# Optimization experiments

Measured on AMD Instinct MI355X. Metric: run time of the kernel, lower is better.

## Reference

```python
import jax, jax.numpy as jnp
import numpy as np

B, H, Wd = 32, 64, 64
C_IN = 65            # ambient Lorentz dim (1 time + 64 space)
KH = KW = 3          # kernel
OUT = 256            # out_channels (ambient); linear space dim = 255
HCAT = (C_IN - 1) * KH * KW + 1  # 577
CURV = 1.0


def setup_inputs() -> dict:
    key = jax.random.key(0)
    k1, k2, k3 = jax.random.split(key, 3)
    # spatial (tangent-like) components, projected onto the hyperboloid
    v = jax.random.normal(k1, (B, H, Wd, C_IN - 1), dtype=jnp.float32) * 0.5
    t = jnp.sqrt(1.0 / CURV + jnp.sum(v * v, axis=-1, keepdims=True))
    x = jnp.concatenate([t, v], axis=-1)  # valid Lorentz points, (B,H,W,65)
    W = jax.random.normal(k2, (OUT - 1, HCAT), dtype=jnp.float32) * (1.0 / np.sqrt(HCAT))
    b = jnp.zeros((OUT - 1,), dtype=jnp.float32)
    return {"x": x, "W": W, "b": b}


def reference(x, W, b):
    c = CURV
    Bn, Hn, Wn, C = x.shape
    # 'SAME' padding with stride 1, kernel 3 -> pad 1 on each side, edge mode
    xp = jnp.pad(x, ((0, 0), (1, 1), (1, 1), (0, 0)), mode="edge")
    # im2col: stack the KH*KW shifted views -> (B, H, W, N, C)
    slabs = [xp[:, i:i + Hn, j:j + Wn, :] for i in range(KH) for j in range(KW)]
    patches = jnp.stack(slabs, axis=3)
    N = KH * KW
    # Lorentz direct concatenation (HCat):
    # time = sqrt(sum_i t_i^2 - (N-1)/c), space = concat of spatial parts
    t_cat = jnp.sqrt(jnp.sum(patches[..., 0] ** 2, axis=-1) - (N - 1) / c)
    sp = patches[..., 1:].reshape(Bn, Hn, Wn, N * (C - 1))
    h = jnp.concatenate([t_cat[..., None], sp], axis=-1)  # (B,H,W,577)
    # Hyperbolic linear (Lorentz fully-connected): space part is affine map,
    # time part restores the Lorentz constraint <y,y>_L = -1/c
    z = jnp.einsum("bhwi,oi->bhwo", h, W) + b  # (B,H,W,255)
    t_out = jnp.sqrt(1.0 / c + jnp.sum(z * z, axis=-1, keepdims=True))
    return jnp.concatenate([t_out, z], axis=-1)  # (B,H,W,256)
```

## Files before the change

kernel.cpp:

```cpp
#include <hip/hip_runtime.h>
#include <hip/hip_bf16.h>


#define CLAMP63(v) ((v) < 0 ? 0 : ((v) > 63 ? 63 : (v)))

typedef __attribute__((ext_vector_type(8))) short short8;
typedef __attribute__((ext_vector_type(4))) float floatx4;

__device__ __forceinline__ void gl2lds16(const void* g, void* l) {
  __builtin_amdgcn_global_load_lds(
      (const __attribute__((address_space(1))) void*)g,
      (__attribute__((address_space(3))) void*)l, 16, 0, 0);
}

__global__ void prep_x(const float* __restrict__ x, __hip_bfloat16* __restrict__ xs,
                       float* __restrict__ tsq) {
  int idx = blockIdx.x * 256 + threadIdx.x;
  int p = idx >> 3, g = idx & 7;
  const float* src = x + (size_t)p * 65 + 1 + g * 8;
  __align__(16) __hip_bfloat16 tmp[8];
#pragma unroll
  for (int i = 0; i < 8; ++i) tmp[i] = __float2bfloat16(src[i]);
  *(short8*)(xs + (size_t)idx * 8) = *(const short8*)tmp;
  if (g == 0) { float t = x[(size_t)p * 65]; tsq[p] = t * t; }
}

__global__ void prep_w(const float* __restrict__ W, const float* __restrict__ b,
                       __hip_bfloat16* __restrict__ Wb, float* __restrict__ Wt0,
                       float* __restrict__ bp) {
  int n = blockIdx.x;
  for (int k = threadIdx.x; k < 576; k += 256)
    Wb[n * 576 + k] = __float2bfloat16((n < 255) ? W[n * 577 + 1 + k] : 0.f);
  if (threadIdx.x == 0) {
    Wt0[n] = (n < 255) ? W[n * 577] : 0.f;
    bp[n]  = (n < 255) ? b[n] : 0.f;
  }
}

#define STAGE(IT, BUF)                                                          \
  do {                                                                          \
    const int nbr_ = (IT) >> 1;                                                 \
    const int dy_ = nbr_ / 3 - 1, dx_ = nbr_ % 3 - 1;                           \
    const int c0_ = ((IT) & 1) * 32;                                            \
    int y2_ = CLAMP63(a_by + dy_);                                              \
    int x2_ = CLAMP63(a_bx + dx_);                                              \
    gl2lds16(xs + (size_t)((a_bb * 64 + y2_) * 64 + x2_) * 64 + c0_ + a_kg * 8, \
             Ab + (BUF) * 4096 + w * 512);                                      \
    _Pragma("unroll")                                                           \
    for (int j = 0; j < 2; ++j)                                                 \
      gl2lds16(b_src[j] + (IT) * 32, Bb + (BUF) * 8192 + (w * 2 + j) * 512);    \
  } while (0)

__launch_bounds__(512, 4)
__global__ void hypconv_main(const float* __restrict__ tsq,
                             const __hip_bfloat16* __restrict__ xs,
                             const __hip_bfloat16* __restrict__ Wb,
                             const float* __restrict__ Wt0,
                             const float* __restrict__ bp,
                             float* __restrict__ out) {
  __shared__ __align__(16) char smem[49152];
  __shared__ float tc_lds[128];
  ushort* Ab = (ushort*)smem;
  ushort* Bb = (ushort*)(smem + 16384);
  float* zbuf = (float*)smem;

  const int tid = threadIdx.x;
  const int w = tid >> 6, lane = tid & 63;
  const int quad = lane >> 4, ln = lane & 15;
  const int pix_base = blockIdx.x * 128;
  const int m_off = (w >> 2) * 64, n_off = (w & 3) * 64;

  const int a_kg = w >> 1;
  int apix = pix_base + (w & 1) * 64 + lane;
  const int a_bx = apix & 63, a_by = (apix >> 6) & 63, a_bb = apix >> 12;
  const __hip_bfloat16* b_src[2];
#pragma unroll
  for (int j = 0; j < 2; ++j) {
    int c = w * 2 + j;
    b_src[j] = Wb + (size_t)((c & 3) * 64 + lane) * 576 + (c >> 2) * 8;
  }

  floatx4 acc[4][4];
#pragma unroll
  for (int mf = 0; mf < 4; ++mf)
#pragma unroll
    for (int nf = 0; nf < 4; ++nf)
      acc[mf][nf] = (floatx4){0.f, 0.f, 0.f, 0.f};

  STAGE(0, 0);

  if (tid < 128) {
    int pix = pix_base + tid;
    int bx = pix & 63, by = (pix >> 6) & 63, bb = pix >> 12;
    float s = 0.f;
#pragma unroll
    for (int dy = -1; dy <= 1; ++dy) {
      int y2 = CLAMP63(by + dy);
#pragma unroll
      for (int dx = -1; dx <= 1; ++dx) {
        int x2 = CLAMP63(bx + dx);
        s += tsq[(bb * 64 + y2) * 64 + x2];
      }
    }
    tc_lds[tid] = sqrtf(s - 8.0f);
  }

  for (int it = 0; it < 18; ++it) {
    __syncthreads();
    if (it < 17) STAGE(it + 1, (it + 1) & 1);
    const ushort* Ar = Ab + (it & 1) * 4096;
    const ushort* Br = Bb + (it & 1) * 8192;
    short8 af[4], bfr[4];
#pragma unroll
    for (int mf = 0; mf < 4; ++mf)
      af[mf] = *(const short8*)&Ar[(quad * 128 + m_off + mf * 16 + ln) * 8];
#pragma unroll
    for (int nf = 0; nf < 4; ++nf)
      bfr[nf] = *(const short8*)&Br[(quad * 256 + n_off + nf * 16 + ln) * 8];
#pragma unroll
    for (int mf = 0; mf < 4; ++mf)
#pragma unroll
      for (int nf = 0; nf < 4; ++nf)
        acc[mf][nf] = __builtin_amdgcn_mfma_f32_16x16x32_bf16(af[mf], bfr[nf], acc[mf][nf], 0, 0, 0);
  }

  __syncthreads();
  float wn[4], bnv[4];
#pragma unroll
  for (int nf = 0; nf < 4; ++nf) {
    int n = n_off + nf * 16 + ln;
    wn[nf] = Wt0[n];
    bnv[nf] = bp[n];
  }

#pragma unroll
  for (int mf = 0; mf < 4; ++mf) {
#pragma unroll
    for (int r = 0; r < 4; ++r) {
      float tcv = tc_lds[m_off + mf * 16 + quad * 4 + r];
      int lr = (w >> 2) * 16 + quad * 4 + r;
#pragma unroll
      for (int nf = 0; nf < 4; ++nf) {
        float z = acc[mf][nf][r] + bnv[nf] + tcv * wn[nf];
        zbuf[lr * 260 + ((1 + n_off + nf * 16 + ln) & 255)] = z;
      }
    }
    __syncthreads();
#pragma unroll
    for (int rr = 0; rr < 4; ++rr) {
      int lr = w * 4 + rr;
      float4 v = *(const float4*)&zbuf[lr * 260 + lane * 4];
      float ss = v.x * v.x + v.y * v.y + v.z * v.z + v.w * v.w;
      ss += __shfl_xor(ss, 1, 64);
      ss += __shfl_xor(ss, 2, 64);
      ss += __shfl_xor(ss, 4, 64);
      ss += __shfl_xor(ss, 8, 64);
      ss += __shfl_xor(ss, 16, 64);
      ss += __shfl_xor(ss, 32, 64);
      float tout = sqrtf(1.0f + ss);
      if (lane == 0) v.x = tout;
      int m = (lr >> 4) * 64 + mf * 16 + (lr & 15);
      *(float4*)&out[(size_t)(pix_base + m) * 256 + lane * 4] = v;
    }
    if (mf < 3) __syncthreads();
  }
}

extern "C" void kernel_launch(void* const* d_in, const int* in_sizes, int n_in,
                              void* d_out, int out_size, void* d_ws, size_t ws_size,
                              hipStream_t stream) {
  const float* x = (const float*)d_in[0];
  const float* W = (const float*)d_in[1];
  const float* b = (const float*)d_in[2];
  float* out = (float*)d_out;
  char* ws = (char*)d_ws;

  __hip_bfloat16* xs  = (__hip_bfloat16*)(ws);
  __hip_bfloat16* Wb  = (__hip_bfloat16*)(ws + 16777216);
  float*          Wt0 = (float*)(ws + 17072128);
  float*          bp  = (float*)(ws + 17073152);
  float*          tsq = (float*)(ws + 17074176);

  prep_x<<<4096, 256, 0, stream>>>(x, xs, tsq);
  prep_w<<<256,  256, 0, stream>>>(W, b, Wb, Wt0, bp);
  hypconv_main<<<1024, 512, 0, stream>>>(tsq, xs, Wb, Wt0, bp, out);
}
```

Before: 221.5 us.

## Fuse input bf16 conversion into main kernel with LDS halo tile

Removes the separate prep_x pass. Each block now loads a 4x66 halo of x straight from global memory, converts it to bf16 and stores it in LDS with an XOR swizzle, so the nine stencil neighbours are read from LDS and not re-fetched from global per iteration. The time-component sums also come from the LDS halo. It additionally remaps block order, shifts W rows by one so the output column layout needs no wrap, and lowers occupancy to 2 blocks per CU because LDS use grows. In exchange there are uncoalesced fp32 reads of 65-float rows and a larger LDS footprint per block.

```diff
diff --git a/kernel.cpp b/kernel.cpp
--- a/kernel.cpp
+++ b/kernel.cpp
@@ -13,66 +13,47 @@
       (__attribute__((address_space(3))) void*)l, 16, 0, 0);
 }
 
-__global__ void prep_x(const float* __restrict__ x, __hip_bfloat16* __restrict__ xs,
-                       float* __restrict__ tsq) {
-  int idx = blockIdx.x * 256 + threadIdx.x;
-  int p = idx >> 3, g = idx & 7;
-  const float* src = x + (size_t)p * 65 + 1 + g * 8;
-  __align__(16) __hip_bfloat16 tmp[8];
-#pragma unroll
-  for (int i = 0; i < 8; ++i) tmp[i] = __float2bfloat16(src[i]);
-  *(short8*)(xs + (size_t)idx * 8) = *(const short8*)tmp;
-  if (g == 0) { float t = x[(size_t)p * 65]; tsq[p] = t * t; }
-}
-
 __global__ void prep_w(const float* __restrict__ W, const float* __restrict__ b,
                        __hip_bfloat16* __restrict__ Wb, float* __restrict__ Wt0,
                        float* __restrict__ bp) {
   int n = blockIdx.x;
   for (int k = threadIdx.x; k < 576; k += 256)
-    Wb[n * 576 + k] = __float2bfloat16((n < 255) ? W[n * 577 + 1 + k] : 0.f);
+    Wb[n * 576 + k] = __float2bfloat16((n >= 1) ? W[(n - 1) * 577 + 1 + k] : 0.f);
   if (threadIdx.x == 0) {
-    Wt0[n] = (n < 255) ? W[n * 577] : 0.f;
-    bp[n]  = (n < 255) ? b[n] : 0.f;
+    Wt0[n] = (n >= 1) ? W[(n - 1) * 577] : 0.f;
+    bp[n]  = (n >= 1) ? b[n - 1] : 0.f;
   }
 }
 
-#define STAGE(IT, BUF)                                                          \
-  do {                                                                          \
-    const int nbr_ = (IT) >> 1;                                                 \
-    const int dy_ = nbr_ / 3 - 1, dx_ = nbr_ % 3 - 1;                           \
-    const int c0_ = ((IT) & 1) * 32;                                            \
-    int y2_ = CLAMP63(a_by + dy_);                                              \
-    int x2_ = CLAMP63(a_bx + dx_);                                              \
-    gl2lds16(xs + (size_t)((a_bb * 64 + y2_) * 64 + x2_) * 64 + c0_ + a_kg * 8, \
-             Ab + (BUF) * 4096 + w * 512);                                      \
-    _Pragma("unroll")                                                           \
-    for (int j = 0; j < 2; ++j)                                                 \
-      gl2lds16(b_src[j] + (IT) * 32, Bb + (BUF) * 8192 + (w * 2 + j) * 512);    \
+#define STAGE_B(IT, BUF)                                                          \
+  do {                                                                            \
+    _Pragma("unroll")                                                             \
+    for (int j_ = 0; j_ < 2; ++j_)                                                \
+      gl2lds16(b_src[j_] + (IT) * 32, Bb + (BUF) * 8192 + (w * 2 + j_) * 512);    \
   } while (0)
 
-__launch_bounds__(512, 4)
-__global__ void hypconv_main(const float* __restrict__ tsq,
-                             const __hip_bfloat16* __restrict__ xs,
+__launch_bounds__(512, 2)
+__global__ void hypconv_main(const float* __restrict__ x,
                              const __hip_bfloat16* __restrict__ Wb,
                              const float* __restrict__ Wt0,
                              const float* __restrict__ bp,
                              float* __restrict__ out) {
-  __shared__ __align__(16) char smem[49152];
+  __shared__ __align__(16) char smem[67616];
   __shared__ float tc_lds[128];
-  ushort* Ab = (ushort*)smem;
-  ushort* Bb = (ushort*)(smem + 16384);
+  float* ts = (float*)(smem + 33792);
+  ushort* Bb = (ushort*)(smem + 34848);
   float* zbuf = (float*)smem;
 
   const int tid = threadIdx.x;
   const int w = tid >> 6, lane = tid & 63;
   const int quad = lane >> 4, ln = lane & 15;
-  const int pix_base = blockIdx.x * 128;
+
+  const int mb = ((blockIdx.x & 7) << 7) + (blockIdx.x >> 3);
+  const int pix_base = mb * 128;
+  const int bb = mb >> 5;
+  const int r0 = (mb & 31) << 1;
   const int m_off = (w >> 2) * 64, n_off = (w & 3) * 64;
 
-  const int a_kg = w >> 1;
-  int apix = pix_base + (w & 1) * 64 + lane;
-  const int a_bx = apix & 63, a_by = (apix >> 6) & 63, a_bb = apix >> 12;
   const __hip_bfloat16* b_src[2];
 #pragma unroll
   for (int j = 0; j < 2; ++j) {
@@ -87,33 +68,54 @@
     for (int nf = 0; nf < 4; ++nf)
       acc[mf][nf] = (floatx4){0.f, 0.f, 0.f, 0.f};
 
-  STAGE(0, 0);
+  STAGE_B(0, 0);
+
+  for (int t = tid; t < 528; t += 512) {
+    const int hp = t >> 1, h = t & 1;
+    const int hyi = hp / 66, hxj = hp - hyi * 66;
+    const int gy = CLAMP63(r0 - 1 + hyi);
+    const int gx = CLAMP63(hxj - 1);
+    const float* row = x + (size_t)((bb << 12) + (gy << 6) + gx) * 65;
+    if (h == 0) { float tv = row[0]; ts[hp] = tv * tv; }
+    const float* sp = row + 1 + h * 32;
+#pragma unroll
+    for (int q = 0; q < 4; ++q) {
+      const int cg = h * 4 + q;
+      __align__(16) __hip_bfloat16 tmp[8];
+#pragma unroll
+      for (int i = 0; i < 8; ++i) tmp[i] = __float2bfloat16(sp[q * 8 + i]);
+      *(short8*)(smem + hp * 128 + ((cg ^ (hp & 7)) << 4)) = *(const short8*)tmp;
+    }
+  }
+  __syncthreads();
 
   if (tid < 128) {
-    int pix = pix_base + tid;
-    int bx = pix & 63, by = (pix >> 6) & 63, bb = pix >> 12;
+    const int ri = tid >> 6, cm = tid & 63;
     float s = 0.f;
 #pragma unroll
-    for (int dy = -1; dy <= 1; ++dy) {
-      int y2 = CLAMP63(by + dy);
+    for (int i = 0; i < 3; ++i)
 #pragma unroll
-      for (int dx = -1; dx <= 1; ++dx) {
-        int x2 = CLAMP63(bx + dx);
-        s += tsq[(bb * 64 + y2) * 64 + x2];
-      }
-    }
+      for (int j = 0; j < 3; ++j)
+        s += ts[(ri + i) * 66 + cm + j];
     tc_lds[tid] = sqrtf(s - 8.0f);
   }
 
+  const int rowterm = (1 + (w >> 2)) * 66 + 1 + ln;
+#pragma unroll
   for (int it = 0; it < 18; ++it) {
     __syncthreads();
-    if (it < 17) STAGE(it + 1, (it + 1) & 1);
-    const ushort* Ar = Ab + (it & 1) * 4096;
+    if (it < 17) STAGE_B(it + 1, (it + 1) & 1);
+    const int nbr = it >> 1;
+    const int dy = nbr / 3 - 1, dx = nbr % 3 - 1;
+    const int c4 = (it & 1) * 4 + quad;
+    const int pb = rowterm + dy * 66 + dx;
     const ushort* Br = Bb + (it & 1) * 8192;
     short8 af[4], bfr[4];
 #pragma unroll
-    for (int mf = 0; mf < 4; ++mf)
-      af[mf] = *(const short8*)&Ar[(quad * 128 + m_off + mf * 16 + ln) * 8];
+    for (int mf = 0; mf < 4; ++mf) {
+      const int pix = pb + mf * 16;
+      af[mf] = *(const short8*)(smem + pix * 128 + ((c4 ^ (pix & 7)) << 4));
+    }
 #pragma unroll
     for (int nf = 0; nf < 4; ++nf)
       bfr[nf] = *(const short8*)&Br[(quad * 256 + n_off + nf * 16 + ln) * 8];
@@ -142,7 +144,7 @@
 #pragma unroll
       for (int nf = 0; nf < 4; ++nf) {
         float z = acc[mf][nf][r] + bnv[nf] + tcv * wn[nf];
-        zbuf[lr * 260 + ((1 + n_off + nf * 16 + ln) & 255)] = z;
+        zbuf[lr * 260 + n_off + nf * 16 + ln] = z;
       }
     }
     __syncthreads();
@@ -175,13 +177,10 @@
   float* out = (float*)d_out;
   char* ws = (char*)d_ws;
 
-  __hip_bfloat16* xs  = (__hip_bfloat16*)(ws);
-  __hip_bfloat16* Wb  = (__hip_bfloat16*)(ws + 16777216);
-  float*          Wt0 = (float*)(ws + 17072128);
-  float*          bp  = (float*)(ws + 17073152);
-  float*          tsq = (float*)(ws + 17074176);
+  __hip_bfloat16* Wb  = (__hip_bfloat16*)(ws);
+  float*          Wt0 = (float*)(ws + 294912);
+  float*          bp  = (float*)(ws + 295936);
 
-  prep_x<<<4096, 256, 0, stream>>>(x, xs, tsq);
-  prep_w<<<256,  256, 0, stream>>>(W, b, Wb, Wt0, bp);
-  hypconv_main<<<1024, 512, 0, stream>>>(tsq, xs, Wb, Wt0, bp, out);
+  prep_w<<<256, 256, 0, stream>>>(W, b, Wb, Wt0, bp);
+  hypconv_main<<<1024, 512, 0, stream>>>(x, Wb, Wt0, bp, out);
 }
```

Result: slower. 231.9 us (+4.7%).

## Load A fragments directly from global memory, drop A LDS staging, swizzle blocks

Applied to the files above, without the earlier changes.

The activation (A) operand now goes straight from global memory into registers each iteration instead of being staged through LDS. This cuts the LDS footprint from about 48KB to 33KB, and the launch-bounds occupancy hint rises from 4 to 8. The block index is remapped so consecutive blocks land on different row groups, and the K loop is fully unrolled with the x-neighbour offsets precomputed. The risk is that global-load latency now sits directly on the MFMA critical path, since those loads are not prefetched a stage ahead.

```diff
diff --git a/kernel.cpp b/kernel.cpp
--- a/kernel.cpp
+++ b/kernel.cpp
@@ -37,42 +37,44 @@
   }
 }
 
-#define STAGE(IT, BUF)                                                          \
+#define STAGE_B(IT, BUF)                                                        \
   do {                                                                          \
-    const int nbr_ = (IT) >> 1;                                                 \
-    const int dy_ = nbr_ / 3 - 1, dx_ = nbr_ % 3 - 1;                           \
-    const int c0_ = ((IT) & 1) * 32;                                            \
-    int y2_ = CLAMP63(a_by + dy_);                                              \
-    int x2_ = CLAMP63(a_bx + dx_);                                              \
-    gl2lds16(xs + (size_t)((a_bb * 64 + y2_) * 64 + x2_) * 64 + c0_ + a_kg * 8, \
-             Ab + (BUF) * 4096 + w * 512);                                      \
     _Pragma("unroll")                                                           \
-    for (int j = 0; j < 2; ++j)                                                 \
-      gl2lds16(b_src[j] + (IT) * 32, Bb + (BUF) * 8192 + (w * 2 + j) * 512);    \
+    for (int j_ = 0; j_ < 2; ++j_)                                              \
+      gl2lds16(b_src[j_] + (IT) * 32, Bb + (BUF) * 8192 + (w * 2 + j_) * 512);  \
   } while (0)
 
-__launch_bounds__(512, 4)
+__launch_bounds__(512, 8)
 __global__ void hypconv_main(const float* __restrict__ tsq,
                              const __hip_bfloat16* __restrict__ xs,
                              const __hip_bfloat16* __restrict__ Wb,
                              const float* __restrict__ Wt0,
                              const float* __restrict__ bp,
                              float* __restrict__ out) {
-  __shared__ __align__(16) char smem[49152];
-  __shared__ float tc_lds[128];
-  ushort* Ab = (ushort*)smem;
-  ushort* Bb = (ushort*)(smem + 16384);
-  float* zbuf = (float*)smem;
+  __shared__ __align__(16) char smem[33792];
+  float* tc_lds = (float*)smem;
+  ushort* Bb = (ushort*)(smem + 512);
+  float* zbuf = (float*)(smem + 512);
 
   const int tid = threadIdx.x;
   const int w = tid >> 6, lane = tid & 63;
   const int quad = lane >> 4, ln = lane & 15;
-  const int pix_base = blockIdx.x * 128;
+
+  const int mb = ((blockIdx.x & 7) << 7) + (blockIdx.x >> 3);
+  const int pix_base = mb * 128;
   const int m_off = (w >> 2) * 64, n_off = (w & 3) * 64;
 
-  const int a_kg = w >> 1;
-  int apix = pix_base + (w & 1) * 64 + lane;
-  const int a_bx = apix & 63, a_by = (apix >> 6) & 63, a_bb = apix >> 12;
+  const int bb = mb >> 5;
+  const int a_by = ((mb & 31) << 1) + (w >> 2);
+  int a_px[4][3];
+#pragma unroll
+  for (int mf = 0; mf < 4; ++mf)
+#pragma unroll
+    for (int dxi = 0; dxi < 3; ++dxi) {
+      int x2 = CLAMP63(mf * 16 + ln + dxi - 1);
+      a_px[mf][dxi] = ((bb << 12) + x2) << 6;
+    }
+
   const __hip_bfloat16* b_src[2];
 #pragma unroll
   for (int j = 0; j < 2; ++j) {
@@ -87,11 +89,11 @@
     for (int nf = 0; nf < 4; ++nf)
       acc[mf][nf] = (floatx4){0.f, 0.f, 0.f, 0.f};
 
-  STAGE(0, 0);
+  STAGE_B(0, 0);
 
   if (tid < 128) {
     int pix = pix_base + tid;
-    int bx = pix & 63, by = (pix >> 6) & 63, bb = pix >> 12;
+    int bx = pix & 63, by = (pix >> 6) & 63, bb2 = pix >> 12;
     float s = 0.f;
 #pragma unroll
     for (int dy = -1; dy <= 1; ++dy) {
@@ -99,21 +101,25 @@
 #pragma unroll
       for (int dx = -1; dx <= 1; ++dx) {
         int x2 = CLAMP63(bx + dx);
-        s += tsq[(bb * 64 + y2) * 64 + x2];
+        s += tsq[(bb2 * 64 + y2) * 64 + x2];
       }
     }
     tc_lds[tid] = sqrtf(s - 8.0f);
   }
 
+#pragma unroll
   for (int it = 0; it < 18; ++it) {
     __syncthreads();
-    if (it < 17) STAGE(it + 1, (it + 1) & 1);
-    const ushort* Ar = Ab + (it & 1) * 4096;
+    if (it < 17) STAGE_B(it + 1, (it + 1) & 1);
+    const int nbr = it >> 1;
+    const int dy = nbr / 3 - 1, dxi = nbr % 3;
+    const int y2 = CLAMP63(a_by + dy);
+    const int kofs = (it & 1) * 32 + quad * 8;
     const ushort* Br = Bb + (it & 1) * 8192;
     short8 af[4], bfr[4];
 #pragma unroll
     for (int mf = 0; mf < 4; ++mf)
-      af[mf] = *(const short8*)&Ar[(quad * 128 + m_off + mf * 16 + ln) * 8];
+      af[mf] = *(const short8*)(xs + (size_t)(a_px[mf][dxi] + (y2 << 12) + kofs));
 #pragma unroll
     for (int nf = 0; nf < 4; ++nf)
       bfr[nf] = *(const short8*)&Br[(quad * 256 + n_off + nf * 16 + ln) * 8];
```

Result: slower. 863.9 us (+290.1%).
